# Optimization experiments

Measured on AMD Instinct MI355X. Metric: run time of the kernel, lower is better.

Reference implementation:

```python
import jax, jax.numpy as jnp
import numpy as np

N = 25000      # nodes
E = 400000     # edges
D = 128        # num_hidden (per-head out dim)
H = 3          # heads
NEG_SLOPE = 0.2
BN_EPS = 1e-5


def _gatv2(x, edge_index, Wl, bl, Wr, br, att, bias):
    """PyG GATv2Conv (concat=True, add_self_loops=True, dropout=0).
    x: [N, Din]; Wl/Wr: [Din, H*D]; att: [H, D]; bias: [H*D].
    """
    n = x.shape[0]
    h, d = att.shape
    loops = jnp.arange(n)
    src = jnp.concatenate([edge_index[0], loops])  # [E+N]
    dst = jnp.concatenate([edge_index[1], loops])
    xl = (x @ Wl + bl).reshape(n, h, d)  # source transform
    xr = (x @ Wr + br).reshape(n, h, d)  # target transform
    # edge scores: a^T LeakyReLU(xl_j + xr_i)
    e = jax.nn.leaky_relu(xl[src] + xr[dst], NEG_SLOPE)   # [E+N, H, D]
    score = jnp.einsum('ehd,hd->eh', e, att)              # [E+N, H]
    # segment softmax over incoming edges of each dst node
    m = jax.ops.segment_max(score, dst, num_segments=n)   # [N, H]
    ex = jnp.exp(score - m[dst])
    denom = jax.ops.segment_sum(ex, dst, num_segments=n)  # [N, H]
    alpha = ex / denom[dst]                               # [E+N, H]
    out = jax.ops.segment_sum(alpha[:, :, None] * xl[src], dst, num_segments=n)
    return out.reshape(n, h * d) + bias                   # [N, H*D]


def _batchnorm(x, gamma, beta):
    mu = jnp.mean(x, axis=0)
    var = jnp.var(x, axis=0)  # biased, as torch BN uses for normalization
    return gamma * (x - mu) * jax.lax.rsqrt(var + BN_EPS) + beta


def setup_inputs() -> dict:
    key = jax.random.key(0)
    ks = iter(jax.random.split(key, 32))
    s = 0.1
    p = {}
    p['x'] = jax.random.normal(next(ks), (N, D), jnp.float32)
    p['edge_index'] = jax.random.randint(next(ks), (2, E), 0, N, jnp.int64)
    for i in (1, 2):
        p[f'Wl{i}'] = s * jax.random.normal(next(ks), (D, H * D), jnp.float32)
        p[f'bl{i}'] = jnp.zeros((H * D,), jnp.float32)
        p[f'Wr{i}'] = s * jax.random.normal(next(ks), (D, H * D), jnp.float32)
        p[f'br{i}'] = jnp.zeros((H * D,), jnp.float32)
        p[f'att{i}'] = s * jax.random.normal(next(ks), (H, D), jnp.float32)
        p[f'bc{i}'] = jnp.zeros((H * D,), jnp.float32)
        p[f'g{i}'] = jnp.ones((D,), jnp.float32)
        p[f'be{i}'] = jnp.zeros((D,), jnp.float32)
    p['W1'] = s * jax.random.normal(next(ks), (H * D, D), jnp.float32)
    p['b1'] = jnp.zeros((D,), jnp.float32)
    p['W2'] = s * jax.random.normal(next(ks), (2 * H * D, D), jnp.float32)
    p['b2'] = jnp.zeros((D,), jnp.float32)
    return p


def reference(x, edge_index, Wl1, bl1, Wr1, br1, att1, bc1, g1, be1,
              Wl2, bl2, Wr2, br2, att2, bc2, g2, be2, W1, b1, W2, b2):
    x_in = _gatv2(x, edge_index, Wl1, bl1, Wr1, br1, att1, bc1)  # [N, H*D]
    h = _batchnorm(x_in @ W1 + b1, g1, be1)
    h = jax.nn.relu(h)                                           # [N, D]
    h2 = _gatv2(h, edge_index, Wl2, bl2, Wr2, br2, att2, bc2)    # [N, H*D]
    out = jnp.concatenate([h2, x_in], axis=1) @ W2 + b2          # [N, D]
    out = _batchnorm(out, g2, be2)
    return jax.nn.relu(out)
```

## Files before the change

kernel.cpp:

```cpp
#include <hip/hip_runtime.h>
#include <math.h>

#define NN 25000
#define NE 400000
#define DD 128
#define HD 384
#define NEG 0.2f
#define EPS 1e-5f

typedef unsigned int u32;
typedef unsigned short u16;
typedef __attribute__((ext_vector_type(8))) short short8;
typedef __attribute__((ext_vector_type(4))) float floatx4;

__device__ __forceinline__ u32 bf16_1(float x) {
    u32 u = __float_as_uint(x);
    return (u + 0x7fffu + ((u >> 16) & 1u)) >> 16;
}
__device__ __forceinline__ float blo(u32 u) { return __uint_as_float(u << 16); }
__device__ __forceinline__ float bhi(u32 u) { return __uint_as_float(u & 0xffff0000u); }

__device__ __forceinline__ void up8(uint4 u, float* f) {
    f[0] = blo(u.x); f[1] = bhi(u.x); f[2] = blo(u.y); f[3] = bhi(u.y);
    f[4] = blo(u.z); f[5] = bhi(u.z); f[6] = blo(u.w); f[7] = bhi(u.w);
}


__global__ void k_scan1(const int* __restrict__ cnt, int* __restrict__ bsum) {
    __shared__ int sh[256];
    int i = blockIdx.x * 256 + threadIdx.x;
    sh[threadIdx.x] = (i < NN) ? (cnt[i] + 1) : 0;
    __syncthreads();
    for (int o = 128; o >= 1; o >>= 1) {
        if ((int)threadIdx.x < o) sh[threadIdx.x] += sh[threadIdx.x + o];
        __syncthreads();
    }
    if (threadIdx.x == 0) bsum[blockIdx.x] = sh[0];
}

__global__ void k_scan2(int* __restrict__ bsum, int nblk) {
    __shared__ int sh[128];
    int v = ((int)threadIdx.x < nblk) ? bsum[threadIdx.x] : 0;
    sh[threadIdx.x] = v;
    __syncthreads();
    for (int o = 1; o < 128; o <<= 1) {
        int t = (threadIdx.x >= (unsigned)o) ? sh[threadIdx.x - o] : 0;
        __syncthreads();
        sh[threadIdx.x] += t;
        __syncthreads();
    }
    if ((int)threadIdx.x < nblk) bsum[threadIdx.x] = sh[threadIdx.x];
}

__global__ void k_scan3(const int* __restrict__ cnt, const int* __restrict__ bsum,
                        int* __restrict__ row_ptr, int* __restrict__ col_src,
                        int* __restrict__ cur) {
    __shared__ int sh[256];
    int i = blockIdx.x * 256 + threadIdx.x;
    int v = (i < NN) ? (cnt[i] + 1) : 0;
    sh[threadIdx.x] = v;
    __syncthreads();
    for (int o = 1; o < 256; o <<= 1) {
        int t = (threadIdx.x >= (unsigned)o) ? sh[threadIdx.x - o] : 0;
        __syncthreads();
        sh[threadIdx.x] += t;
        __syncthreads();
    }
    int base = blockIdx.x ? bsum[blockIdx.x - 1] : 0;
    if (i < NN) {
        int incl = base + sh[threadIdx.x];
        row_ptr[i + 1] = incl;
        int p = incl - v;
        col_src[p] = i;
        cur[i] = p + 1;
    }
    if (i == 0) row_ptr[0] = 0;
}

__global__ void k_fill_edges(const int* __restrict__ src, const int* __restrict__ dst,
                             int* __restrict__ cur, int* __restrict__ col_src) {
    int e = blockIdx.x * 256 + threadIdx.x;
    if (e < NE) { int p = atomicAdd(&cur[dst[e]], 1); col_src[p] = src[e]; }
}

__global__ void k_cast_all(const float* __restrict__ x,
                           const float* __restrict__ Wl1, const float* __restrict__ Wr1,
                           const float* __restrict__ W1,
                           const float* __restrict__ Wl2, const float* __restrict__ Wr2,
                           const float* __restrict__ W2,
                           const float* __restrict__ bl1, const float* __restrict__ br1,
                           const float* __restrict__ bl2, const float* __restrict__ br2,
                           const int* __restrict__ edst,
                           u16* __restrict__ xb, u16* __restrict__ WfT1,
                           u16* __restrict__ W1T, u16* __restrict__ WfT2,
                           u16* __restrict__ W2T,
                           float* __restrict__ fb1, float* __restrict__ fb2,
                           int* __restrict__ cnt, float* __restrict__ stats) {
    int i = blockIdx.x * 256 + threadIdx.x;
    if (i < 400000) {
        const float4* xp = (const float4*)(x + (size_t)i * 8);
        float4 a = xp[0], b = xp[1];
        uint4 w;
        w.x = bf16_1(a.x) | (bf16_1(a.y) << 16);
        w.y = bf16_1(a.z) | (bf16_1(a.w) << 16);
        w.z = bf16_1(b.x) | (bf16_1(b.y) << 16);
        w.w = bf16_1(b.z) | (bf16_1(b.w) << 16);
        *(uint4*)(xb + (size_t)i * 8) = w;
        return;
    }
    i -= 400000;
    if (i < 400000) { atomicAdd(&cnt[edst[i]], 1); return; }
    i -= 400000;
    if (i < 49152) { int k = i / 384, n = i - k * 384; WfT1[n * 128 + k] = (u16)bf16_1(Wl1[i]); return; }
    i -= 49152;
    if (i < 49152) { int k = i / 384, n = i - k * 384; WfT1[(384 + n) * 128 + k] = (u16)bf16_1(Wr1[i]); return; }
    i -= 49152;
    if (i < 49152) { int k = i / 128, n = i - k * 128; W1T[n * 384 + k] = (u16)bf16_1(W1[i]); return; }
    i -= 49152;
    if (i < 49152) { int k = i / 384, n = i - k * 384; WfT2[n * 128 + k] = (u16)bf16_1(Wl2[i]); return; }
    i -= 49152;
    if (i < 49152) { int k = i / 384, n = i - k * 384; WfT2[(384 + n) * 128 + k] = (u16)bf16_1(Wr2[i]); return; }
    i -= 49152;
    if (i < 98304) { int k = i / 128, n = i - k * 128; W2T[n * 768 + k] = (u16)bf16_1(W2[i]); return; }
    i -= 98304;
    if (i < 768) { fb1[i] = (i < 384) ? bl1[i] : br1[i - 384]; return; }
    i -= 768;
    if (i < 768) { fb2[i] = (i < 384) ? bl2[i] : br2[i - 384]; return; }
    i -= 768;
    if (i < 512) stats[i] = 0.f;
}
#define CAST_TOTAL (400000 + 400000 + 5 * 49152 + 98304 + 1536 + 512)

__global__ __launch_bounds__(256) void k_gemm_k128(
        const u16* __restrict__ A, const u16* __restrict__ BT,
        const float* __restrict__ bias, u16* __restrict__ Cb, int M) {
    __shared__ short sA[128 * 128];
    __shared__ short sB[128 * 128];
    int tid = threadIdx.x;
    int wv = tid >> 6, lane = tid & 63;
    int quad = lane >> 4, m16 = lane & 15;
    int mb = blockIdx.y * 128, nb = blockIdx.x * 128;

#pragma unroll
    for (int j = 0; j < 8; ++j) {
        int L = j * 256 + tid;
        int r = L >> 4, c8 = (L & 15) ^ (r & 15);
        int gr = mb + r; gr = gr < M ? gr : M - 1;
        __builtin_amdgcn_global_load_lds(
            (const __attribute__((address_space(1))) void*)(A + (size_t)gr * 128 + c8 * 8),
            (__attribute__((address_space(3))) void*)(sA + (size_t)L * 8), 16, 0, 0);
    }
#pragma unroll
    for (int j = 0; j < 8; ++j) {
        int L = j * 256 + tid;
        int r = L >> 4, c8 = (L & 15) ^ (r & 15);
        __builtin_amdgcn_global_load_lds(
            (const __attribute__((address_space(1))) void*)(BT + (size_t)(nb + r) * 128 + c8 * 8),
            (__attribute__((address_space(3))) void*)(sB + (size_t)L * 8), 16, 0, 0);
    }
    __syncthreads();

    floatx4 acc[2][8];
#pragma unroll
    for (int mf = 0; mf < 2; ++mf)
#pragma unroll
        for (int nf = 0; nf < 8; ++nf)
#pragma unroll
            for (int r = 0; r < 4; ++r) acc[mf][nf][r] = 0.f;

#pragma unroll
    for (int ks = 0; ks < 4; ++ks) {
        int slot = (ks * 4 + quad) ^ m16;
        int row0 = wv * 32 + m16, row1 = row0 + 16;
        short8 a0 = *(const short8*)(sA + ((size_t)row0 * 16 + slot) * 8);
        short8 a1 = *(const short8*)(sA + ((size_t)row1 * 16 + slot) * 8);
#pragma unroll
        for (int nf = 0; nf < 8; ++nf) {
            short8 b = *(const short8*)(sB + ((size_t)(nf * 16 + m16) * 16 + slot) * 8);
            acc[0][nf] = __builtin_amdgcn_mfma_f32_16x16x32_bf16(a0, b, acc[0][nf], 0, 0, 0);
            acc[1][nf] = __builtin_amdgcn_mfma_f32_16x16x32_bf16(a1, b, acc[1][nf], 0, 0, 0);
        }
    }
    __syncthreads();

#pragma unroll
    for (int mf = 0; mf < 2; ++mf)
#pragma unroll
        for (int nf = 0; nf < 8; ++nf)
#pragma unroll
            for (int r = 0; r < 4; ++r) {
                int row = wv * 32 + mf * 16 + quad * 4 + r;
                int col = nf * 16 + m16;
                sA[row * 128 + col] = (short)bf16_1(acc[mf][nf][r] + bias[nb + col]);
            }
    __syncthreads();
    int xr = nb >= 384;
    int h = (xr ? (nb - 384) : nb) >> 7;
    u16* cb = Cb + ((size_t)(xr * 3 + h) * NN) * 128;
#pragma unroll
    for (int i = 0; i < 8; ++i) {
        int u = i * 256 + tid;
        int row = u >> 4, c8 = u & 15;
        int grow = mb + row;
        if (grow < M)
            *(uint4*)(cb + (size_t)grow * 128 + c8 * 8) = *(const uint4*)(sA + (size_t)u * 8);
    }
}

__global__ __launch_bounds__(256) void k_gemm_bf(
        const u16* __restrict__ A, const u16* __restrict__ BT,
        const float* __restrict__ bias,
        float* __restrict__ Cf, float* __restrict__ stats,
        int M, int N, int K, int lda) {
    const int NF = 4;
    __shared__ short smem[17408];
    short* sA = smem;
    short* sB = smem + 8192;
    int tid = threadIdx.x;
    int wv = tid >> 6, lane = tid & 63;
    int quad = lane >> 4, m16 = lane & 15;
    int sw = m16 & 7;
    int mb = blockIdx.y * 128, nb = blockIdx.x * 64;

    floatx4 acc[2][NF];
#pragma unroll
    for (int mf = 0; mf < 2; ++mf)
#pragma unroll
        for (int nf = 0; nf < NF; ++nf)
#pragma unroll
            for (int r = 0; r < 4; ++r) acc[mf][nf][r] = 0.f;

    for (int k0 = 0; k0 < K; k0 += 64) {
#pragma unroll
        for (int j = 0; j < 4; ++j) {
            int L = (wv * 4 + j) * 64 + lane;
            int r = L >> 3, c8 = (L & 7) ^ (r & 7);
            int gr = mb + r; gr = gr < M ? gr : M - 1;
            __builtin_amdgcn_global_load_lds(
                (const __attribute__((address_space(1))) void*)(A + (size_t)gr * lda + k0 + c8 * 8),
                (__attribute__((address_space(3))) void*)(sA + (size_t)(wv * 4 + j) * 512),
                16, 0, 0);
        }
#pragma unroll
        for (int j = 0; j < 2; ++j) {
            int L = (wv * 2 + j) * 64 + lane;
            int r = L >> 3, c8 = (L & 7) ^ (r & 7);
            __builtin_amdgcn_global_load_lds(
                (const __attribute__((address_space(1))) void*)(BT + (size_t)(nb + r) * K + k0 + c8 * 8),
                (__attribute__((address_space(3))) void*)(sB + (size_t)(wv * 2 + j) * 512),
                16, 0, 0);
        }
        __syncthreads();
#pragma unroll
        for (int ks = 0; ks < 2; ++ks) {
            int t = (ks * 4 + quad) ^ sw;
            const short* pa = sA + t * 8;
            const short* pb = sB + t * 8;
            short8 a0 = *(const short8*)(pa + (wv * 32 + m16) * 64);
            short8 a1 = *(const short8*)(pa + (wv * 32 + 16 + m16) * 64);
#pragma unroll
            for (int nf = 0; nf < NF; ++nf) {
                short8 b = *(const short8*)(pb + (nf * 16 + m16) * 64);
                acc[0][nf] = __builtin_amdgcn_mfma_f32_16x16x32_bf16(a0, b, acc[0][nf], 0, 0, 0);
                acc[1][nf] = __builtin_amdgcn_mfma_f32_16x16x32_bf16(a1, b, acc[1][nf], 0, 0, 0);
            }
        }
        __syncthreads();
    }
    float* fs = (float*)smem;
#pragma unroll
    for (int mf = 0; mf < 2; ++mf)
#pragma unroll
        for (int nf = 0; nf < NF; ++nf)
#pragma unroll
            for (int r = 0; r < 4; ++r) {
                int row = wv * 32 + mf * 16 + quad * 4 + r;
                int col = nf * 16 + m16;
                fs[row * 64 + col] = acc[mf][nf][r] + (bias ? bias[nb + col] : 0.f);
            }
    __syncthreads();
#pragma unroll
    for (int i = 0; i < 8; ++i) {
        int u = i * 256 + tid;
        int row = u >> 4, c4 = u & 15;
        int grow = mb + row;
        if (grow < M)
            *(float4*)(Cf + (size_t)grow * N + nb + c4 * 4) = *(const float4*)(fs + (size_t)u * 4);
    }
    if (stats) {
        float* ps = (float*)(smem + 16384);
        int col = tid & 63, qr = tid >> 6;
        int vr = M - mb; vr = vr < 128 ? vr : 128;
        int r0 = qr * 32, r1 = r0 + 32 < vr ? r0 + 32 : vr;
        float s = 0.f, q = 0.f;
        for (int r = r0; r < r1; ++r) { float v = fs[r * 64 + col]; s += v; q += v * v; }
        ps[qr * 64 + col] = s;
        ps[256 + qr * 64 + col] = q;
        __syncthreads();
        if (tid < 64) {
            float ss = ps[tid] + ps[64 + tid] + ps[128 + tid] + ps[192 + tid];
            atomicAdd(&stats[nb + tid], ss);
        } else if (tid < 128) {
            int c = tid - 64;
            float qq = ps[256 + c] + ps[320 + c] + ps[384 + c] + ps[448 + c];
            atomicAdd(&stats[128 + nb + c], qq);
        }
    }
}

__global__ __launch_bounds__(256) void k_gat_h(const u32* __restrict__ XLb,
                                               const u32* __restrict__ XRb,
                                               const float* __restrict__ att,
                                               const float* __restrict__ bias,
                                               const int* __restrict__ row_ptr,
                                               const int* __restrict__ col_src,
                                               u32* __restrict__ outb, int nbase) {
    int h = blockIdx.y;
    const u32* XLh = XLb + (size_t)h * NN * 64;
    const u32* XRh = XRb + (size_t)h * NN * 64;
    int node = nbase + blockIdx.x * 4 + (threadIdx.x >> 6);
    int lane = threadIdx.x & 63;
    int g = lane >> 4, gl = lane & 15;

    float xr_f[8], att_f[8], acc[8];
    up8(*(const uint4*)(XRh + (size_t)node * 64 + 4 * gl), xr_f);
    *(float4*)&att_f[0] = *(const float4*)&att[h * 128 + 8 * gl];
    *(float4*)&att_f[4] = *(const float4*)&att[h * 128 + 8 * gl + 4];
#pragma unroll
    for (int k = 0; k < 8; ++k) acc[k] = 0.f;
    float l = 0.f;

    int e0 = row_ptr[node];
    int cntE = row_ptr[node + 1] - e0;
    int elast = e0 + cntE - 1;

    int ea = e0 + g;     ea = ea < elast ? ea : elast;
    int eb = e0 + g + 4; eb = eb < elast ? eb : elast;
    uint4 ua = *(const uint4*)(XLh + (size_t)col_src[ea] * 64 + 4 * gl);
    uint4 ub = *(const uint4*)(XLh + (size_t)col_src[eb] * 64 + 4 * gl);

    for (int t = g; t < cntE; t += 8) {
        int e2 = e0 + t + 8;  e2 = e2 < elast ? e2 : elast;
        int e3 = e0 + t + 12; e3 = e3 < elast ? e3 : elast;
        uint4 un0 = *(const uint4*)(XLh + (size_t)col_src[e2] * 64 + 4 * gl);
        uint4 un1 = *(const uint4*)(XLh + (size_t)col_src[e3] * 64 + 4 * gl);

        float xa[8], xb[8];
        up8(ua, xa); up8(ub, xb);
        float pa = 0.f, pb = 0.f;
#pragma unroll
        for (int k = 0; k < 8; ++k) {
            float va = xa[k] + xr_f[k];
            float vb = xb[k] + xr_f[k];
            pa = fmaf(fmaxf(va, NEG * va), att_f[k], pa);
            pb = fmaf(fmaxf(vb, NEG * vb), att_f[k], pb);
        }
#pragma unroll
        for (int o = 1; o <= 8; o <<= 1) {
            pa += __shfl_xor(pa, o);
            pb += __shfl_xor(pb, o);
        }
        float wa = __expf(pa);
        float wb = ((t + 4) < cntE) ? __expf(pb) : 0.f;
        l += wa + wb;
#pragma unroll
        for (int k = 0; k < 8; ++k)
            acc[k] = fmaf(wa, xa[k], fmaf(wb, xb[k], acc[k]));

        ua = un0; ub = un1;
    }

#pragma unroll
    for (int o = 16; o <= 32; o <<= 1) {
        l += __shfl_xor(l, o);
#pragma unroll
        for (int k = 0; k < 8; ++k) acc[k] += __shfl_xor(acc[k], o);
    }

    if (g == 0) {
        float r = 1.f / l;
        float bv[8];
        *(float4*)&bv[0] = *(const float4*)&bias[h * 128 + 8 * gl];
        *(float4*)&bv[4] = *(const float4*)&bias[h * 128 + 8 * gl + 4];
        uint4 w;
        w.x = bf16_1(fmaf(acc[0], r, bv[0])) | (bf16_1(fmaf(acc[1], r, bv[1])) << 16);
        w.y = bf16_1(fmaf(acc[2], r, bv[2])) | (bf16_1(fmaf(acc[3], r, bv[3])) << 16);
        w.z = bf16_1(fmaf(acc[4], r, bv[4])) | (bf16_1(fmaf(acc[5], r, bv[5])) << 16);
        w.w = bf16_1(fmaf(acc[6], r, bv[6])) | (bf16_1(fmaf(acc[7], r, bv[7])) << 16);
        *(uint4*)(outb + (size_t)node * 384 + h * 64 + 4 * gl) = w;
    }
}

__global__ void k_bn_apply(float* __restrict__ y, const float* __restrict__ stats,
                           const float* __restrict__ g, const float* __restrict__ be,
                           u16* __restrict__ yb, int wf) {
    int i = blockIdx.x * 256 + threadIdx.x;
    if (i >= NN * DD / 8) return;
    int idx = i * 8;
    int c0 = idx & 127;
    float v[8];
    *(float4*)&v[0] = *(const float4*)(y + idx);
    *(float4*)&v[4] = *(const float4*)(y + idx + 4);
    const float minv = 1.f / (float)NN;
#pragma unroll
    for (int k = 0; k < 8; ++k) {
        int c = c0 + k;
        float mu = stats[c] * minv;
        float var = stats[128 + c] * minv - mu * mu;
        float sc = g[c] * rsqrtf(var + EPS);
        float sh = be[c] - mu * sc;
        v[k] = fmaxf(fmaf(v[k], sc, sh), 0.f);
    }
    if (wf) {
        *(float4*)(y + idx) = *(const float4*)&v[0];
        *(float4*)(y + idx + 4) = *(const float4*)&v[4];
    }
    if (yb) {
        uint4 w;
        w.x = bf16_1(v[0]) | (bf16_1(v[1]) << 16);
        w.y = bf16_1(v[2]) | (bf16_1(v[3]) << 16);
        w.z = bf16_1(v[4]) | (bf16_1(v[5]) << 16);
        w.w = bf16_1(v[6]) | (bf16_1(v[7]) << 16);
        *(uint4*)(yb + idx) = w;
    }
}


extern "C" void kernel_launch(void* const* d_in, const int* in_sizes, int n_in,
                              void* d_out, int out_size, void* d_ws, size_t ws_size,
                              hipStream_t stream) {
    const float* x    = (const float*)d_in[0];
    const int*   ei   = (const int*)d_in[1];
    const float* Wl1  = (const float*)d_in[2];
    const float* bl1  = (const float*)d_in[3];
    const float* Wr1  = (const float*)d_in[4];
    const float* br1  = (const float*)d_in[5];
    const float* att1 = (const float*)d_in[6];
    const float* bc1  = (const float*)d_in[7];
    const float* g1   = (const float*)d_in[8];
    const float* be1  = (const float*)d_in[9];
    const float* Wl2  = (const float*)d_in[10];
    const float* bl2  = (const float*)d_in[11];
    const float* Wr2  = (const float*)d_in[12];
    const float* br2  = (const float*)d_in[13];
    const float* att2 = (const float*)d_in[14];
    const float* bc2  = (const float*)d_in[15];
    const float* g2   = (const float*)d_in[16];
    const float* be2  = (const float*)d_in[17];
    const float* W1   = (const float*)d_in[18];
    const float* b1   = (const float*)d_in[19];
    const float* W2   = (const float*)d_in[20];
    const float* b2   = (const float*)d_in[21];
    const int* esrc = ei;
    const int* edst = ei + NE;
    float* out = (float*)d_out;

    float* bufD   = (float*)d_ws;
    float* stats  = bufD + 3200000;
    int* row_ptr  = (int*)(stats + 512);
    int* cnt      = row_ptr + 25002;
    int* col_src  = cnt + 25000;
    int* bsum     = col_src + 425000;
    float* fb1    = (float*)(bsum + 132);
    float* fb2    = fb1 + 768;
    u16* xb       = (u16*)(fb2 + 768);
    u16* XLb      = xb + 3200000;
    u16* XRb      = XLb + 3 * NN * 128;
    u16* bufCat   = XRb + 3 * NN * 128;
    u16* bufDb    = bufCat + 19200000;
    u16* WfT1     = bufDb + 3200000;
    u16* W1T      = WfT1 + 98304;
    u16* WfT2     = W1T + 49152;
    u16* W2T      = WfT2 + 98304;

    hipMemsetAsync(cnt, 0, NN * sizeof(int), stream);
    k_cast_all<<<(CAST_TOTAL + 255) / 256, 256, 0, stream>>>(
        x, Wl1, Wr1, W1, Wl2, Wr2, W2, bl1, br1, bl2, br2, edst,
        xb, WfT1, W1T, WfT2, W2T, fb1, fb2, cnt, stats);

    k_scan1<<<98, 256, 0, stream>>>(cnt, bsum);
    k_scan2<<<1, 128, 0, stream>>>(bsum, 98);
    k_scan3<<<98, 256, 0, stream>>>(cnt, bsum, row_ptr, col_src, cnt);
    k_fill_edges<<<(NE + 255) / 256, 256, 0, stream>>>(esrc, edst, cnt, col_src);

    dim3 blk(256);
    dim3 gK(6, (NN + 127) / 128);
    dim3 g128(2, (NN + 127) / 128);
    dim3 gGatH(NN / 8, 3);

    k_gemm_k128<<<gK, blk, 0, stream>>>(xb, WfT1, fb1, XLb, NN);
    k_gat_h<<<gGatH, blk, 0, stream>>>((const u32*)XLb, (const u32*)XRb, att1, bc1,
                                       row_ptr, col_src, (u32*)bufCat + 192, 0);
    k_gat_h<<<gGatH, blk, 0, stream>>>((const u32*)XLb, (const u32*)XRb, att1, bc1,
                                       row_ptr, col_src, (u32*)bufCat + 192, NN / 2);

    k_gemm_bf<<<g128, blk, 0, stream>>>(bufCat + 384, W1T, b1, bufD, stats, NN, DD, HD, 768);
    k_bn_apply<<<(NN * DD / 8 + 255) / 256, 256, 0, stream>>>(bufD, stats, g1, be1, bufDb, 0);

    k_gemm_k128<<<gK, blk, 0, stream>>>(bufDb, WfT2, fb2, XLb, NN);
    k_gat_h<<<gGatH, blk, 0, stream>>>((const u32*)XLb, (const u32*)XRb, att2, bc2,
                                       row_ptr, col_src, (u32*)bufCat, 0);
    k_gat_h<<<gGatH, blk, 0, stream>>>((const u32*)XLb, (const u32*)XRb, att2, bc2,
                                       row_ptr, col_src, (u32*)bufCat, NN / 2);

    k_gemm_bf<<<g128, blk, 0, stream>>>(bufCat, W2T, b2, out, stats + 256, NN, DD, 768, 768);
    k_bn_apply<<<(NN * DD / 8 + 255) / 256, 256, 0, stream>>>(out, stats + 256, g2, be2, nullptr, 1);
}
```

Baseline: 396.2 us.

## Fold scan2 into scan3, merge GAT launches, shrink output GEMM M-tile to 64

Three unrelated launch-level changes. The single-block scan2 kernel is removed and every scan3 block now redoes the 98-entry block-sum prefix scan in shared memory, which saves one launch at the cost of repeated work. The two half-range k_gat_h launches per layer become one launch over all nodes. The narrow-output k_gemm_bf moves from 128-row to 64-row tiles with one 16-row MFMA strip per wave, doubling the block count to fill more CUs, though each B tile is reused across fewer rows.

Result: no change. 390.5 us (-1.4%).

```diff
diff --git a/kernel.cpp b/kernel.cpp
--- a/kernel.cpp
+++ b/kernel.cpp
@@ -38,37 +38,33 @@
     if (threadIdx.x == 0) bsum[blockIdx.x] = sh[0];
 }
 
-__global__ void k_scan2(int* __restrict__ bsum, int nblk) {
-    __shared__ int sh[128];
-    int v = ((int)threadIdx.x < nblk) ? bsum[threadIdx.x] : 0;
-    sh[threadIdx.x] = v;
-    __syncthreads();
-    for (int o = 1; o < 128; o <<= 1) {
-        int t = (threadIdx.x >= (unsigned)o) ? sh[threadIdx.x - o] : 0;
-        __syncthreads();
-        sh[threadIdx.x] += t;
-        __syncthreads();
-    }
-    if ((int)threadIdx.x < nblk) bsum[threadIdx.x] = sh[threadIdx.x];
-}
-
 __global__ void k_scan3(const int* __restrict__ cnt, const int* __restrict__ bsum,
                         int* __restrict__ row_ptr, int* __restrict__ col_src,
                         int* __restrict__ cur) {
     __shared__ int sh[256];
-    int i = blockIdx.x * 256 + threadIdx.x;
+    __shared__ int sb[128];
+    int tid = threadIdx.x;
+    if (tid < 128) sb[tid] = (tid < 98) ? bsum[tid] : 0;
+    __syncthreads();
+    for (int o = 1; o < 128; o <<= 1) {
+        int t = (tid >= o && tid < 128) ? sb[tid - o] : 0;
+        __syncthreads();
+        if (tid < 128) sb[tid] += t;
+        __syncthreads();
+    }
+    int i = blockIdx.x * 256 + tid;
     int v = (i < NN) ? (cnt[i] + 1) : 0;
-    sh[threadIdx.x] = v;
+    sh[tid] = v;
     __syncthreads();
     for (int o = 1; o < 256; o <<= 1) {
-        int t = (threadIdx.x >= (unsigned)o) ? sh[threadIdx.x - o] : 0;
-        __syncthreads();
-        sh[threadIdx.x] += t;
-        __syncthreads();
-    }
-    int base = blockIdx.x ? bsum[blockIdx.x - 1] : 0;
+        int t = (tid >= o) ? sh[tid - o] : 0;
+        __syncthreads();
+        sh[tid] += t;
+        __syncthreads();
+    }
+    int base = blockIdx.x ? sb[blockIdx.x - 1] : 0;
     if (i < NN) {
-        int incl = base + sh[threadIdx.x];
+        int incl = base + sh[tid];
         row_ptr[i + 1] = incl;
         int p = incl - v;
         col_src[p] = i;
@@ -212,43 +208,38 @@
         const float* __restrict__ bias,
         float* __restrict__ Cf, float* __restrict__ stats,
         int M, int N, int K, int lda) {
-    const int NF = 4;
-    __shared__ short smem[17408];
+    __shared__ short smem[9216];
     short* sA = smem;
-    short* sB = smem + 8192;
+    short* sB = smem + 4096;
     int tid = threadIdx.x;
     int wv = tid >> 6, lane = tid & 63;
     int quad = lane >> 4, m16 = lane & 15;
     int sw = m16 & 7;
-    int mb = blockIdx.y * 128, nb = blockIdx.x * 64;
-
-    floatx4 acc[2][NF];
-#pragma unroll
-    for (int mf = 0; mf < 2; ++mf)
-#pragma unroll
-        for (int nf = 0; nf < NF; ++nf)
-#pragma unroll
-            for (int r = 0; r < 4; ++r) acc[mf][nf][r] = 0.f;
+    int mb = blockIdx.y * 64, nb = blockIdx.x * 64;
+
+    floatx4 acc[4];
+#pragma unroll
+    for (int nf = 0; nf < 4; ++nf)
+#pragma unroll
+        for (int r = 0; r < 4; ++r) acc[nf][r] = 0.f;
 
     for (int k0 = 0; k0 < K; k0 += 64) {
 #pragma unroll
-        for (int j = 0; j < 4; ++j) {
-            int L = (wv * 4 + j) * 64 + lane;
+        for (int j = 0; j < 2; ++j) {
+            int L = j * 256 + tid;
             int r = L >> 3, c8 = (L & 7) ^ (r & 7);
             int gr = mb + r; gr = gr < M ? gr : M - 1;
             __builtin_amdgcn_global_load_lds(
                 (const __attribute__((address_space(1))) void*)(A + (size_t)gr * lda + k0 + c8 * 8),
-                (__attribute__((address_space(3))) void*)(sA + (size_t)(wv * 4 + j) * 512),
-                16, 0, 0);
+                (__attribute__((address_space(3))) void*)(sA + (size_t)L * 8), 16, 0, 0);
         }
 #pragma unroll
         for (int j = 0; j < 2; ++j) {
-            int L = (wv * 2 + j) * 64 + lane;
+            int L = j * 256 + tid;
             int r = L >> 3, c8 = (L & 7) ^ (r & 7);
             __builtin_amdgcn_global_load_lds(
                 (const __attribute__((address_space(1))) void*)(BT + (size_t)(nb + r) * K + k0 + c8 * 8),
-                (__attribute__((address_space(3))) void*)(sB + (size_t)(wv * 2 + j) * 512),
-                16, 0, 0);
+                (__attribute__((address_space(3))) void*)(sB + (size_t)L * 8), 16, 0, 0);
         }
         __syncthreads();
 #pragma unroll
@@ -256,31 +247,27 @@
             int t = (ks * 4 + quad) ^ sw;
             const short* pa = sA + t * 8;
             const short* pb = sB + t * 8;
-            short8 a0 = *(const short8*)(pa + (wv * 32 + m16) * 64);
-            short8 a1 = *(const short8*)(pa + (wv * 32 + 16 + m16) * 64);
-#pragma unroll
-            for (int nf = 0; nf < NF; ++nf) {
+            short8 a0 = *(const short8*)(pa + (wv * 16 + m16) * 64);
+#pragma unroll
+            for (int nf = 0; nf < 4; ++nf) {
                 short8 b = *(const short8*)(pb + (nf * 16 + m16) * 64);
-                acc[0][nf] = __builtin_amdgcn_mfma_f32_16x16x32_bf16(a0, b, acc[0][nf], 0, 0, 0);
-                acc[1][nf] = __builtin_amdgcn_mfma_f32_16x16x32_bf16(a1, b, acc[1][nf], 0, 0, 0);
+                acc[nf] = __builtin_amdgcn_mfma_f32_16x16x32_bf16(a0, b, acc[nf], 0, 0, 0);
             }
         }
         __syncthreads();
     }
     float* fs = (float*)smem;
 #pragma unroll
-    for (int mf = 0; mf < 2; ++mf)
-#pragma unroll
-        for (int nf = 0; nf < NF; ++nf)
-#pragma unroll
-            for (int r = 0; r < 4; ++r) {
-                int row = wv * 32 + mf * 16 + quad * 4 + r;
-                int col = nf * 16 + m16;
-                fs[row * 64 + col] = acc[mf][nf][r] + (bias ? bias[nb + col] : 0.f);
-            }
-    __syncthreads();
-#pragma unroll
-    for (int i = 0; i < 8; ++i) {
+    for (int nf = 0; nf < 4; ++nf)
+#pragma unroll
+        for (int r = 0; r < 4; ++r) {
+            int row = wv * 16 + quad * 4 + r;
+            int col = nf * 16 + m16;
+            fs[row * 64 + col] = acc[nf][r] + (bias ? bias[nb + col] : 0.f);
+        }
+    __syncthreads();
+#pragma unroll
+    for (int i = 0; i < 4; ++i) {
         int u = i * 256 + tid;
         int row = u >> 4, c4 = u & 15;
         int grow = mb + row;
@@ -288,10 +275,10 @@
             *(float4*)(Cf + (size_t)grow * N + nb + c4 * 4) = *(const float4*)(fs + (size_t)u * 4);
     }
     if (stats) {
-        float* ps = (float*)(smem + 16384);
+        float* ps = (float*)(smem + 8192);
         int col = tid & 63, qr = tid >> 6;
-        int vr = M - mb; vr = vr < 128 ? vr : 128;
-        int r0 = qr * 32, r1 = r0 + 32 < vr ? r0 + 32 : vr;
+        int vr = M - mb; vr = vr < 64 ? vr : 64;
+        int r0 = qr * 16, r1 = r0 + 16 < vr ? r0 + 16 : vr;
         float s = 0.f, q = 0.f;
         for (int r = r0; r < r1; ++r) { float v = fs[r * 64 + col]; s += v; q += v * v; }
         ps[qr * 64 + col] = s;
@@ -314,11 +301,11 @@
                                                const float* __restrict__ bias,
                                                const int* __restrict__ row_ptr,
                                                const int* __restrict__ col_src,
-                                               u32* __restrict__ outb, int nbase) {
+                                               u32* __restrict__ outb) {
     int h = blockIdx.y;
     const u32* XLh = XLb + (size_t)h * NN * 64;
     const u32* XRh = XRb + (size_t)h * NN * 64;
-    int node = nbase + blockIdx.x * 4 + (threadIdx.x >> 6);
+    int node = blockIdx.x * 4 + (threadIdx.x >> 6);
     int lane = threadIdx.x & 63;
     int g = lane >> 4, gl = lane & 15;
 
@@ -479,30 +466,25 @@
         xb, WfT1, W1T, WfT2, W2T, fb1, fb2, cnt, stats);
 
     k_scan1<<<98, 256, 0, stream>>>(cnt, bsum);
-    k_scan2<<<1, 128, 0, stream>>>(bsum, 98);
     k_scan3<<<98, 256, 0, stream>>>(cnt, bsum, row_ptr, col_src, cnt);
     k_fill_edges<<<(NE + 255) / 256, 256, 0, stream>>>(esrc, edst, cnt, col_src);
 
     dim3 blk(256);
     dim3 gK(6, (NN + 127) / 128);
-    dim3 g128(2, (NN + 127) / 128);
-    dim3 gGatH(NN / 8, 3);
+    dim3 g64(2, (NN + 63) / 64);
+    dim3 gGat((NN + 3) / 4, 3);
 
     k_gemm_k128<<<gK, blk, 0, stream>>>(xb, WfT1, fb1, XLb, NN);
-    k_gat_h<<<gGatH, blk, 0, stream>>>((const u32*)XLb, (const u32*)XRb, att1, bc1,
-                                       row_ptr, col_src, (u32*)bufCat + 192, 0);
-    k_gat_h<<<gGatH, blk, 0, stream>>>((const u32*)XLb, (const u32*)XRb, att1, bc1,
-                                       row_ptr, col_src, (u32*)bufCat + 192, NN / 2);
-
-    k_gemm_bf<<<g128, blk, 0, stream>>>(bufCat + 384, W1T, b1, bufD, stats, NN, DD, HD, 768);
+    k_gat_h<<<gGat, blk, 0, stream>>>((const u32*)XLb, (const u32*)XRb, att1, bc1,
+                                      row_ptr, col_src, (u32*)bufCat + 192);
+
+    k_gemm_bf<<<g64, blk, 0, stream>>>(bufCat + 384, W1T, b1, bufD, stats, NN, DD, HD, 768);
     k_bn_apply<<<(NN * DD / 8 + 255) / 256, 256, 0, stream>>>(bufD, stats, g1, be1, bufDb, 0);
 
     k_gemm_k128<<<gK, blk, 0, stream>>>(bufDb, WfT2, fb2, XLb, NN);
-    k_gat_h<<<gGatH, blk, 0, stream>>>((const u32*)XLb, (const u32*)XRb, att2, bc2,
-                                       row_ptr, col_src, (u32*)bufCat, 0);
-    k_gat_h<<<gGatH, blk, 0, stream>>>((const u32*)XLb, (const u32*)XRb, att2, bc2,
-                                       row_ptr, col_src, (u32*)bufCat, NN / 2);
-
-    k_gemm_bf<<<g128, blk, 0, stream>>>(bufCat, W2T, b2, out, stats + 256, NN, DD, 768, 768);
+    k_gat_h<<<gGat, blk, 0, stream>>>((const u32*)XLb, (const u32*)XRb, att2, bc2,
+                                      row_ptr, col_src, (u32*)bufCat);
+
+    k_gemm_bf<<<g64, blk, 0, stream>>>(bufCat, W2T, b2, out, stats + 256, NN, DD, 768, 768);
     k_bn_apply<<<(NN * DD / 8 + 255) / 256, 256, 0, stream>>>(out, stats + 256, g2, be2, nullptr, 1);
 }
```
